# Performance work log

Hardware: AMD Instinct MI355X
Metric: run time of the kernel (lower is better)

The kernel has to match this reference:

```python
import jax, jax.numpy as jnp
import numpy as np

B, H, W, C = 32, 52, 56, 384
WS, SHIFT, NH = 7, 3, 12
HP = H + 4            # padded height (layer_num=0)
HD = C // NH          # head dim = 32
N = WS * WS           # tokens per window = 49
NW = (HP // WS) * (W // WS)  # 64 windows per image
SCALE = HD ** -0.5
DFF = 4 * C


def _np_window_partition(x, ws):
    b, h, w, c = x.shape
    x = x.reshape(b, h // ws, ws, w // ws, ws, c).transpose(0, 1, 3, 2, 4, 5)
    return x.reshape(-1, ws, ws, c)


def _build_masks_and_relidx():
    # relative position index (torch meshgrid default = 'ij')
    coords = np.stack(np.meshgrid(np.arange(WS), np.arange(WS), indexing='ij'))
    cf = coords.reshape(2, -1)
    rc = (cf[:, :, None] - cf[:, None, :]).transpose(1, 2, 0).astype(np.int64)
    rc[:, :, 0] += WS - 1
    rc[:, :, 1] += WS - 1
    rc[:, :, 0] *= 2 * WS - 1
    rel_idx = rc.sum(-1)  # (49, 49)
    # shift attn mask (layer_num=0 -> flag False, H_=H+4, standard slices)
    img = np.zeros((1, HP, W, 1), np.float32)
    sl = (slice(0, -WS), slice(-WS, -SHIFT), slice(-SHIFT, None))
    cnt = 0
    for hs in sl:
        for ws_ in sl:
            img[:, hs, ws_, :] = cnt
            cnt += 1
    mw = _np_window_partition(img, WS).reshape(-1, N)
    am = mw[:, None, :] - mw[:, :, None]
    attn_mask = np.where(am != 0, np.float32(-100.0), np.float32(0.0))
    # pad mask: rows 0:4 marked -10
    pm = np.zeros((1, HP, W, 1), np.float32)
    pm[:, 0:4, :, :] = -10.0
    pw = _np_window_partition(pm, WS).reshape(-1, N)
    pa = pw[:, None, :] + pw[:, :, None]
    pad_mask = np.where(pa != 0, np.float32(-900.0), np.float32(0.0))
    return jnp.asarray(attn_mask), jnp.asarray(pad_mask), jnp.asarray(rel_idx, jnp.int32)


def setup_inputs() -> dict:
    key = jax.random.key(0)
    ks = jax.random.split(key, 8)
    attn_mask, pad_mask, rel_idx = _build_masks_and_relidx()
    s = 0.02
    return {
        'x': jax.random.normal(ks[0], (B, H * W, C), jnp.float32),
        'norm1_g': jnp.ones((C,), jnp.float32),
        'norm1_b': jnp.zeros((C,), jnp.float32),
        'qkv_w': jax.random.normal(ks[1], (C, 3 * C), jnp.float32) * s,
        'qkv_b': jnp.zeros((3 * C,), jnp.float32),
        'rpb_table': jax.random.normal(ks[2], ((2 * WS - 1) ** 2, NH), jnp.float32) * s,
        'proj_w': jax.random.normal(ks[3], (C, C), jnp.float32) * s,
        'proj_b': jnp.zeros((C,), jnp.float32),
        'norm2_g': jnp.ones((C,), jnp.float32),
        'norm2_b': jnp.zeros((C,), jnp.float32),
        'fc1_w': jax.random.normal(ks[4], (C, DFF), jnp.float32) * s,
        'fc1_b': jnp.zeros((DFF,), jnp.float32),
        'fc2_w': jax.random.normal(ks[5], (DFF, C), jnp.float32) * s,
        'fc2_b': jnp.zeros((C,), jnp.float32),
        'attn_mask': attn_mask,
        'pad_mask': pad_mask,
        'rel_idx': rel_idx,
    }


def _ln(x, g, b):
    m = x.mean(-1, keepdims=True)
    v = ((x - m) ** 2).mean(-1, keepdims=True)
    return (x - m) / jnp.sqrt(v + 1e-5) * g + b


def reference(x, norm1_g, norm1_b, qkv_w, qkv_b, rpb_table, proj_w, proj_b,
              norm2_g, norm2_b, fc1_w, fc1_b, fc2_w, fc2_b,
              attn_mask, pad_mask, rel_idx):
    shortcut = x
    h = _ln(x, norm1_g, norm1_b).reshape(B, H, W, C)
    # cyclic shift + top padding of 4 rows (layer_num=0)
    h = jnp.roll(h, (-SHIFT, -SHIFT), (1, 2))
    h = jnp.pad(h, ((0, 0), (4, 0), (0, 0), (0, 0)))
    # window partition -> (B*NW, N, C)
    win = h.reshape(B, HP // WS, WS, W // WS, WS, C).transpose(0, 1, 3, 2, 4, 5).reshape(-1, N, C)
    qkv = (win @ qkv_w + qkv_b).reshape(-1, N, 3, NH, HD).transpose(2, 0, 3, 1, 4)
    q, k, v = qkv[0] * SCALE, qkv[1], qkv[2]  # (B_, NH, N, HD)
    attn = jnp.einsum('bhnd,bhmd->bhnm', q, k)
    bias = rpb_table[rel_idx.reshape(-1)].reshape(N, N, NH).transpose(2, 0, 1)
    attn = attn + bias[None]
    attn = attn.reshape(B, NW, NH, N, N) + pad_mask[None, :, None] + attn_mask[None, :, None]
    attn = jax.nn.softmax(attn.reshape(-1, NH, N, N), axis=-1)
    o = jnp.einsum('bhnm,bhmd->bhnd', attn, v).transpose(0, 2, 1, 3).reshape(-1, N, C)
    o = o @ proj_w + proj_b
    # window reverse, remove pad rows, roll back by 2*shift (block_num==2)
    o = o.reshape(B, HP // WS, W // WS, WS, WS, C).transpose(0, 1, 3, 2, 4, 5).reshape(B, HP, W, C)
    o = o[:, 4:]
    o = jnp.roll(o, (2 * SHIFT, 2 * SHIFT), (1, 2))
    x1 = shortcut + o.reshape(B, H * W, C)
    t = _ln(x1, norm2_g, norm2_b)
    t = jax.nn.gelu(t @ fc1_w + fc1_b, approximate=False) @ fc2_w + fc2_b
    return x1 + t
```

## Files before the change

kernel.cpp:

```cpp
#include <hip/hip_runtime.h>
#include <hip/hip_bf16.h>

typedef unsigned short u16;
typedef short s16x8 __attribute__((ext_vector_type(8)));
typedef float f32x4 __attribute__((ext_vector_type(4)));
typedef __bf16 bf16x8 __attribute__((ext_vector_type(8)));

#define SCALE_F 0.17677669529663687f

#define OFF_CM    ((size_t)0)
#define OFF_WQ    ((size_t)8<<20)
#define OFF_WP    (OFF_WQ + 884736)
#define OFF_W1    (OFF_WP + 294912)
#define OFF_W2    (OFF_W1 + 1179648)
#define OFF_AWIN  ((size_t)12<<20)
#define OFF_OBUF  ((size_t)90<<20)
#define OFF_ARENA ((size_t)168<<20)

#define QKV_FULL  ((size_t)100352*1152*2)
#define FC1_FULL  ((size_t)93184*1536*2)

static __device__ __forceinline__ u16 f2b(float f) {
    unsigned u = __float_as_uint(f);
    u += 0x7fffu + ((u >> 16) & 1u);
    return (u16)(u >> 16);
}
static __device__ __forceinline__ float b2f(u16 u) {
    return __uint_as_float((unsigned)u << 16);
}

union frag_u { s16x8 s; bf16x8 b; };
static __device__ __forceinline__ bf16x8 tob(s16x8 v) { frag_u u; u.s = v; return u.b; }

static __device__ __forceinline__ void mfma_bf16(f32x4& d, s16x8 a, s16x8 b) {
    asm("v_mfma_f32_16x16x32_bf16 %0, %1, %2, %0" : "+v"(d) : "v"(a), "v"(b));
}

static __device__ __forceinline__ void gload16(const void* g, void* l) {
    __builtin_amdgcn_global_load_lds(
        (const __attribute__((address_space(1))) unsigned int*)g,
        (__attribute__((address_space(3))) unsigned int*)l, 16, 0, 0);
}

__global__ void cm_kernel(const float* __restrict__ am, const float* __restrict__ pm,
                          const float* __restrict__ rpb, const int* __restrict__ ridx,
                          float* __restrict__ cmo)
{
    const int wpos = blockIdx.x, head = blockIdx.y;
    float* o = cmo + ((size_t)wpos*12 + head)*2401;
    const float* a = am + (size_t)wpos*2401;
    const float* p = pm + (size_t)wpos*2401;
    for (int e = threadIdx.x; e < 2401; e += 256)
        o[e] = a[e] + p[e] + rpb[ridx[e]*12 + head];
}

__global__ void wconv_kernel(const float* __restrict__ w, u16* __restrict__ wt,
                             int K, int N)
{
    const int k = blockIdx.x*256 + threadIdx.x;
    const int n = blockIdx.y;
    if (k < K) wt[(size_t)n*K + k] = f2b(w[(size_t)k*N + n]);
}

template<int WINDOWED>
__global__ __launch_bounds__(256, 4)
void ln_kernel(const float* __restrict__ x, const float* __restrict__ g,
               const float* __restrict__ bt, u16* __restrict__ out)
{
    const int lane = threadIdx.x & 63;
    const int row = blockIdx.x*4 + (threadIdx.x >> 6);
    u16* orow = out + (size_t)row*384;
    const float* xr;
    if (WINDOWED) {
        const int win = row / 49, n = row - win*49;
        const int wpos = win & 63, b = win >> 6;
        const int n7 = n / 7;
        const int hp = (wpos >> 3)*7 + n7;
        if (hp < 4) {
            #pragma unroll
            for (int j=0;j<6;j++) orow[lane + 64*j] = 0;
            return;
        }
        const int wp = (wpos & 7)*7 + (n - n7*7);
        int h = hp - 1; if (h >= 52) h -= 52;
        int w = wp + 3; if (w >= 56) w -= 56;
        xr = x + (((size_t)b*52 + h)*56 + w)*384;
    } else {
        xr = x + (size_t)row*384;
    }
    float v[6]; float sum = 0.f;
    #pragma unroll
    for (int j=0;j<6;j++){ v[j] = xr[lane + 64*j]; sum += v[j]; }
    #pragma unroll
    for (int m=1;m<64;m<<=1) sum += __shfl_xor(sum, m);
    const float mean = sum * (1.f/384.f);
    float var = 0.f;
    #pragma unroll
    for (int j=0;j<6;j++){ float d = v[j]-mean; var += d*d; }
    #pragma unroll
    for (int m=1;m<64;m<<=1) var += __shfl_xor(var, m);
    const float rstd = rsqrtf(var*(1.f/384.f) + 1e-5f);
    #pragma unroll
    for (int j=0;j<6;j++){
        const int c = lane + 64*j;
        orow[c] = f2b((v[j]-mean)*rstd*g[c] + bt[c]);
    }
}

template<int EPI>
__global__ __launch_bounds__(256, 2)
void gemm_kernel(const u16* __restrict__ A, const u16* __restrict__ Bt,
                 const float* __restrict__ bias, void* __restrict__ outp,
                 const float* __restrict__ extra, int M, int N, int K)
{
    (void)M;
    __shared__ u16 Als[2][4096];
    __shared__ u16 Bls[2][4096];
    const int tid = threadIdx.x;
    const int lane = tid & 63;
    const int wid = tid >> 6;
    const int wr = wid >> 1, wc = wid & 1;
    const int r16 = lane & 15, kc = lane >> 4;

    const int gx = gridDim.x;
    const int nwg = gx * gridDim.y;
    const int flat = blockIdx.y*gx + blockIdx.x;
    const int q8 = nwg >> 3, r8 = nwg & 7;
    const int xcd = flat & 7, idx = flat >> 3;
    const int tile = (xcd < r8 ? xcd*(q8+1) : r8*(q8+1) + (xcd-r8)*q8) + idx;
    const int ty = tile / gx;
    const int m0 = ty*128, n0 = (tile - ty*gx)*128;

    const int srow = tid >> 2, schunk = tid & 3;
    const int nk = K >> 5;

    const u16* Ab = A  + (size_t)(m0 + srow)*K + (schunk ^ ((srow >> 1) & 3))*8;
    const u16* Bb = Bt + (size_t)(n0 + srow)*K + (schunk ^ ((srow >> 1) & 3))*8;
    const size_t rskip = (size_t)64*K;

    gload16(Ab,         &Als[0][tid*8]);
    gload16(Ab + rskip, &Als[0][2048 + tid*8]);
    gload16(Bb,         &Bls[0][tid*8]);
    gload16(Bb + rskip, &Bls[0][2048 + tid*8]);

    f32x4 acc[4][4] = {};
    const int swz = (kc ^ ((r16 >> 1) & 3))*8;
    for (int kt = 0; kt < nk; ++kt) {
        __syncthreads();
        if (kt + 1 < nk) {
            const int buf = (kt + 1) & 1;
            const u16* a = Ab + (kt+1)*32;
            const u16* b = Bb + (kt+1)*32;
            gload16(a,         &Als[buf][tid*8]);
            gload16(a + rskip, &Als[buf][2048 + tid*8]);
            gload16(b,         &Bls[buf][tid*8]);
            gload16(b + rskip, &Bls[buf][2048 + tid*8]);
        }
        const u16* as = Als[kt & 1];
        const u16* bs = Bls[kt & 1];
        s16x8 af[4], bfr[4];
        #pragma unroll
        for (int i=0;i<4;i++) {
            af[i]  = *(const s16x8*)&as[(64*wr + 16*i + r16)*32 + swz];
            bfr[i] = *(const s16x8*)&bs[(64*wc + 16*i + r16)*32 + swz];
        }
        #pragma unroll
        for (int i=0;i<4;i++)
            #pragma unroll
            for (int j=0;j<4;j++)
                mfma_bf16(acc[i][j], af[i], bfr[j]);
    }

    float bj[4];
    #pragma unroll
    for (int j=0;j<4;j++) bj[j] = bias[n0 + 64*wc + 16*j + r16];

    if constexpr (EPI == 0 || EPI == 2) {
        u16* out = (u16*)outp;
        #pragma unroll
        for (int i=0;i<4;i++)
          #pragma unroll
          for (int r=0;r<4;r++) {
            const size_t row = m0 + 64*wr + 16*i + 4*kc + r;
            #pragma unroll
            for (int j=0;j<4;j++) {
                const int col = n0 + 64*wc + 16*j + r16;
                float v = acc[i][j][r] + bj[j];
                if constexpr (EPI == 2) v = 0.5f*v*(1.f + erff(v*0.70710678118f));
                out[row*(size_t)N + col] = f2b(v);
            }
          }
    } else if constexpr (EPI == 3) {
        float* out = (float*)outp;
        #pragma unroll
        for (int i=0;i<4;i++)
          #pragma unroll
          for (int r=0;r<4;r++) {
            const size_t row = m0 + 64*wr + 16*i + 4*kc + r;
            #pragma unroll
            for (int j=0;j<4;j++) {
                const int col = n0 + 64*wc + 16*j + r16;
                out[row*(size_t)N + col] = extra[row*(size_t)N + col] + acc[i][j][r] + bj[j];
            }
          }
    } else {
        float* out = (float*)outp;
        #pragma unroll
        for (int i=0;i<4;i++)
          #pragma unroll
          for (int r=0;r<4;r++) {
            const int row = m0 + 64*wr + 16*i + 4*kc + r;
            const int win = row / 49, n = row - win*49;
            const int wpos = win & 63, b = win >> 6;
            const int n7 = n / 7;
            const int hp = (wpos >> 3)*7 + n7;
            if (hp < 4) continue;
            const int wp = (wpos & 7)*7 + (n - n7*7);
            int h = hp + 2; if (h >= 52) h -= 52;
            int w = wp + 6; if (w >= 56) w -= 56;
            const size_t base = (((size_t)b*52 + h)*56 + w)*384;
            #pragma unroll
            for (int j=0;j<4;j++) {
                const int col = n0 + 64*wc + 16*j + r16;
                out[base + col] = extra[base + col] + acc[i][j][r] + bj[j];
            }
          }
    }
}

__global__ __launch_bounds__(256, 2)
void attn_mfma2(const u16* __restrict__ qkvc, const float* __restrict__ cm,
                u16* __restrict__ o, int win_base)
{
    __shared__ float Sls[4][2432];
    const int tid = threadIdx.x, lane = tid & 63, wv = tid >> 6;
    const int u = blockIdx.x*4 + wv;
    const int wloc = u / 12, head = u - wloc*12;
    const int wglob = win_base + wloc;
    const int wpos = wglob & 63;
    const int r16 = lane & 15, kc = lane >> 4;
    const u16* base = qkvc + (size_t)wloc*49*1152 + head*32;

    bf16x8 qf[4], kf[4];
    #pragma unroll
    for (int i=0;i<4;i++) {
        const int row = 16*i + r16;
        s16x8 qv = {}, kv = {};
        if (row < 49) {
            const u16* p = base + (size_t)row*1152 + kc*8;
            qv = *(const s16x8*)p;
            kv = *(const s16x8*)(p + 384);
        }
        qf[i] = tob(qv); kf[i] = tob(kv);
    }

    float* sw = Sls[wv];
    const float* cmb = cm + ((size_t)wpos*12 + head)*2401;
    #pragma unroll
    for (int i=0;i<4;i++)
      #pragma unroll
      for (int j=0;j<4;j++) {
        f32x4 s = {};
        s = __builtin_amdgcn_mfma_f32_16x16x32_bf16(qf[i], kf[j], s, 0, 0, 0);
        #pragma unroll
        for (int r=0;r<4;r++) {
            const int row = 16*i + 4*kc + r;
            const int col = 16*j + r16;
            if (row < 49 && col < 49)
                sw[row*49 + col] = s[r]*SCALE_F + cmb[row*49 + col];
        }
      }
    __syncthreads();

    float e[49]; float inv = 0.f;
    const int r = lane;
    if (r < 49) {
        #pragma unroll
        for (int c=0;c<49;c++) e[c] = sw[r*49 + c];
        float mx = -1e30f;
        #pragma unroll
        for (int c=0;c<49;c++) mx = fmaxf(mx, e[c]);
        float sm = 0.f;
        #pragma unroll
        for (int c=0;c<49;c++){ e[c] = __expf(e[c]-mx); sm += e[c]; }
        inv = 1.f/sm;
    }
    __syncthreads();

    u16* pw = (u16*)sw;
    if (r < 49) {
        #pragma unroll
        for (int w8 = 0; w8 < 8; ++w8) {
            s16x8 pk = {};
            #pragma unroll
            for (int jj=0;jj<8;jj++) {
                const int c = w8*8 + jj;
                if (c < 49) pk[jj] = (short)f2b(e[c]*inv);
            }
            *(s16x8*)&pw[r*72 + w8*8] = pk;
        }
    }
    __syncthreads();

    bf16x8 vf[2][2];
    const u16* vb = base + 768;
    #pragma unroll
    for (int kk=0;kk<2;kk++)
      #pragma unroll
      for (int jn=0;jn<2;jn++) {
        s16x8 vv;
        #pragma unroll
        for (int jj=0;jj<8;jj++) {
            int k = 32*kk + 8*kc + jj;
            if (k > 48) k = 0;
            vv[jj] = (short)vb[(size_t)k*1152 + 16*jn + r16];
        }
        vf[kk][jn] = tob(vv);
      }

    f32x4 oa[4][2] = {};
    #pragma unroll
    for (int i=0;i<4;i++)
      #pragma unroll
      for (int kk=0;kk<2;kk++) {
        const bf16x8 pa = tob(*(const s16x8*)&pw[(16*i + r16)*72 + 32*kk + kc*8]);
        #pragma unroll
        for (int jn=0;jn<2;jn++)
            oa[i][jn] = __builtin_amdgcn_mfma_f32_16x16x32_bf16(pa, vf[kk][jn], oa[i][jn], 0, 0, 0);
      }

    #pragma unroll
    for (int i=0;i<4;i++)
      #pragma unroll
      for (int rr=0;rr<4;rr++) {
        const int row = 16*i + 4*kc + rr;
        if (row < 49) {
          #pragma unroll
          for (int jn=0;jn<2;jn++)
            o[(size_t)(wglob*49 + row)*384 + head*32 + 16*jn + r16] = f2b(oa[i][jn][rr]);
        }
      }
}

static int pick_chunks(size_t full, size_t avail) {
    for (int n = 1; n <= 8; n <<= 1) if (full / n <= avail) return n;
    return 8;
}

extern "C" void kernel_launch(void* const* d_in, const int* in_sizes, int n_in,
                              void* d_out, int out_size, void* d_ws, size_t ws_size,
                              hipStream_t stream)
{
    (void)in_sizes; (void)n_in; (void)out_size;
    const float* x      = (const float*)d_in[0];
    const float* n1g    = (const float*)d_in[1];
    const float* n1b    = (const float*)d_in[2];
    const float* qkv_w  = (const float*)d_in[3];
    const float* qkv_b  = (const float*)d_in[4];
    const float* rpb    = (const float*)d_in[5];
    const float* proj_w = (const float*)d_in[6];
    const float* proj_b = (const float*)d_in[7];
    const float* n2g    = (const float*)d_in[8];
    const float* n2b    = (const float*)d_in[9];
    const float* fc1_w  = (const float*)d_in[10];
    const float* fc1_b  = (const float*)d_in[11];
    const float* fc2_w  = (const float*)d_in[12];
    const float* fc2_b  = (const float*)d_in[13];
    const float* amask  = (const float*)d_in[14];
    const float* pmask  = (const float*)d_in[15];
    const int*   ridx   = (const int*)d_in[16];

    char* ws = (char*)d_ws;
    float* cm    = (float*)(ws + OFF_CM);
    u16* wqkvT   = (u16*)(ws + OFF_WQ);
    u16* wprojT  = (u16*)(ws + OFF_WP);
    u16* wfc1T   = (u16*)(ws + OFF_W1);
    u16* wfc2T   = (u16*)(ws + OFF_W2);
    u16* awin    = (u16*)(ws + OFF_AWIN);
    u16* obuf    = (u16*)(ws + OFF_OBUF);
    u16* arena   = (u16*)(ws + OFF_ARENA);
    u16* ln2o    = (u16*)(ws + OFF_AWIN);
    float* x1    = (float*)d_out;

    const size_t avail = (ws_size > OFF_ARENA) ? ws_size - OFF_ARENA : 0;

    cm_kernel  <<<dim3(64,12),  256, 0, stream>>>(amask, pmask, rpb, ridx, cm);
    wconv_kernel<<<dim3(2,1152),256, 0, stream>>>(qkv_w,  wqkvT, 384, 1152);
    wconv_kernel<<<dim3(2,384), 256, 0, stream>>>(proj_w, wprojT, 384, 384);
    wconv_kernel<<<dim3(2,1536),256, 0, stream>>>(fc1_w,  wfc1T, 384, 1536);
    wconv_kernel<<<dim3(6,384), 256, 0, stream>>>(fc2_w,  wfc2T, 1536, 384);

    ln_kernel<1><<<25088, 256, 0, stream>>>(x, n1g, n1b, awin);

    {
        const int n_attn = pick_chunks(QKV_FULL, avail);
        const int wchunk = 2048 / n_attn;
        const int rows_a = wchunk * 49;
        for (int c = 0; c < n_attn; ++c) {
            const u16* aA = awin + (size_t)c*rows_a*384;
            gemm_kernel<0><<<dim3(9, rows_a/128), 256, 0, stream>>>(
                aA, wqkvT, qkv_b, arena, nullptr, rows_a, 1152, 384);
            attn_mfma2<<<wchunk*3, 256, 0, stream>>>(arena, cm, obuf, c*wchunk);
        }
    }

    gemm_kernel<1><<<dim3(3,784), 256, 0, stream>>>(obuf, wprojT, proj_b, x1, x, 100352, 384, 384);
    ln_kernel<0><<<23296, 256, 0, stream>>>(x1, n2g, n2b, ln2o);

    {
        const int n_mlp = pick_chunks(FC1_FULL, avail);
        const int rows_m = 93184 / n_mlp;
        for (int c = 0; c < n_mlp; ++c) {
            const size_t ro = (size_t)c*rows_m;
            gemm_kernel<2><<<dim3(12, rows_m/128), 256, 0, stream>>>(
                ln2o + ro*384, wfc1T, fc1_b, arena, nullptr, rows_m, 1536, 384);
            gemm_kernel<3><<<dim3(3, rows_m/128), 256, 0, stream>>>(
                arena, wfc2T, fc2_b, x1 + ro*384, x1 + ro*384, rows_m, 384, 1536);
        }
    }
}
```

Measured before the change: 834.0 us.

## Store QKV head-major per window and use tanh-form GELU in FC1 epilogue

The QKV GEMM epilogue now scatters its output into a per-window, per-(q/k/v, head) contiguous 49x32 layout, so the attention kernel reads Q, K and V rows with a 32-element stride instead of 1152. This aims to give the attention kernel better locality on its loads, at the price of more scattered stores in the GEMM epilogue. Separately, the FC1 GELU switches from erf to a tanh approximation written as a sigmoid with fast exp, which lowers epilogue arithmetic cost but is no longer the exact GELU the reference uses.

```diff
diff --git a/kernel.cpp b/kernel.cpp
--- a/kernel.cpp
+++ b/kernel.cpp
@@ -175,7 +175,28 @@
     #pragma unroll
     for (int j=0;j<4;j++) bj[j] = bias[n0 + 64*wc + 16*j + r16];
 
-    if constexpr (EPI == 0 || EPI == 2) {
+    if constexpr (EPI == 0) {
+        u16* out = (u16*)outp;
+        int colbase[4];
+        #pragma unroll
+        for (int j=0;j<4;j++) {
+            const int col = n0 + 64*wc + 16*j + r16;
+            const int sel = col/384;
+            const int head = (col - sel*384) >> 5;
+            colbase[j] = (sel*12 + head)*1568 + (col & 31);
+        }
+        #pragma unroll
+        for (int i=0;i<4;i++)
+          #pragma unroll
+          for (int r=0;r<4;r++) {
+            const int row = m0 + 64*wr + 16*i + 4*kc + r;
+            const int win = row/49, r49 = row - win*49;
+            u16* dst = out + (size_t)win*56448 + (size_t)r49*32;
+            #pragma unroll
+            for (int j=0;j<4;j++)
+                dst[colbase[j]] = f2b(acc[i][j][r] + bj[j]);
+          }
+    } else if constexpr (EPI == 2) {
         u16* out = (u16*)outp;
         #pragma unroll
         for (int i=0;i<4;i++)
@@ -186,7 +207,8 @@
             for (int j=0;j<4;j++) {
                 const int col = n0 + 64*wc + 16*j + r16;
                 float v = acc[i][j][r] + bj[j];
-                if constexpr (EPI == 2) v = 0.5f*v*(1.f + erff(v*0.70710678118f));
+                const float u2 = v*(0.79788456f + 0.035677408f*v*v);
+                v = v / (1.f + __expf(-2.f*u2));
                 out[row*(size_t)N + col] = f2b(v);
             }
           }
@@ -239,7 +261,9 @@
     const int wglob = win_base + wloc;
     const int wpos = wglob & 63;
     const int r16 = lane & 15, kc = lane >> 4;
-    const u16* base = qkvc + (size_t)wloc*49*1152 + head*32;
+    const u16* bq = qkvc + ((size_t)(wloc*3 + 0)*12 + head)*1568;
+    const u16* bk = qkvc + ((size_t)(wloc*3 + 1)*12 + head)*1568;
+    const u16* bv = qkvc + ((size_t)(wloc*3 + 2)*12 + head)*1568;
 
     bf16x8 qf[4], kf[4];
     #pragma unroll
@@ -247,9 +271,8 @@
         const int row = 16*i + r16;
         s16x8 qv = {}, kv = {};
         if (row < 49) {
-            const u16* p = base + (size_t)row*1152 + kc*8;
-            qv = *(const s16x8*)p;
-            kv = *(const s16x8*)(p + 384);
+            qv = *(const s16x8*)&bq[row*32 + kc*8];
+            kv = *(const s16x8*)&bk[row*32 + kc*8];
         }
         qf[i] = tob(qv); kf[i] = tob(kv);
     }
@@ -303,7 +326,6 @@
     __syncthreads();
 
     bf16x8 vf[2][2];
-    const u16* vb = base + 768;
     #pragma unroll
     for (int kk=0;kk<2;kk++)
       #pragma unroll
@@ -313,7 +335,7 @@
         for (int jj=0;jj<8;jj++) {
             int k = 32*kk + 8*kc + jj;
             if (k > 48) k = 0;
-            vv[jj] = (short)vb[(size_t)k*1152 + 16*jn + r16];
+            vv[jj] = (short)bv[k*32 + 16*jn + r16];
         }
         vf[kk][jn] = tob(vv);
       }
```

Result: no change. 829.1 us (-0.6%).
